# Performance work log

Hardware: AMD Instinct MI355X
Metric: run time of the kernel (lower is better)

The kernel has to match this reference:

```python
import jax, jax.numpy as jnp
import numpy as np

B, S, D = 2, 2048, 1024
H = 16
HD = D // H  # 64


def _xavier(key, shape):
    fan_out, fan_in = shape
    limit = np.sqrt(6.0 / (fan_in + fan_out)).astype(np.float32)
    return jax.random.uniform(key, shape, jnp.float32, -limit, limit)


def setup_inputs() -> dict:
    key = jax.random.key(0)
    ks = jax.random.split(key, 6)
    return {
        "x": jax.random.normal(ks[0], (B, S, D), jnp.float32),
        "pos_bias": jax.random.normal(ks[1], (1, H, S, S), jnp.float32) * 0.02,
        "sinusoidal_pos": jax.random.normal(ks[2], (1, 1, S, HD), jnp.float32),
        "mask": jax.random.randint(ks[3], (1, 1, S, S), 0, 2, jnp.int32),
        "W_qkv": _xavier(ks[4], (3 * D, D)),
        "b_qkv": jnp.zeros((3 * D,), jnp.float32),
        "W_o": _xavier(ks[5], (D, D)),
        "b_o": jnp.zeros((D,), jnp.float32),
    }


def _rotate_half(t):
    # t: [..., HD]; reshape to [..., 2, HD//2], swap halves with sign flip
    t2 = t.reshape(*t.shape[:-1], 2, HD // 2)
    a, b = t2[..., 0, :], t2[..., 1, :]
    return jnp.concatenate((-b, a), axis=-1)


def _apply_rope(t, sinusoidal_pos):
    sp = sinusoidal_pos[:, :, -t.shape[-2]:]
    return t * jnp.cos(sp) + _rotate_half(t) * jnp.sin(sp)


def reference(x, pos_bias, sinusoidal_pos, mask, W_qkv, b_qkv, W_o, b_o):
    b, s, _ = x.shape
    qkv = x @ W_qkv.T + b_qkv                     # [B,S,3D]
    qkv = qkv.reshape(b, s, H, 3 * HD).transpose(0, 2, 1, 3)  # [B,H,S,3hd]
    q, k, v = jnp.split(qkv, 3, axis=-1)
    q = _apply_rope(q, sinusoidal_pos)
    k = _apply_rope(k, sinusoidal_pos)
    logits = jnp.einsum("bhqd,bhkd->bhqk", q, k)  # [B,H,S,S]
    logits = (logits + pos_bias) / np.sqrt(HD).astype(np.float32)
    logits = jnp.where(mask == 0, jnp.float32(-9e15), logits)
    attn = jax.nn.softmax(logits, axis=-1)
    vals = jnp.einsum("bhqk,bhkd->bhqd", attn, v)
    vals = vals.transpose(0, 2, 1, 3).reshape(b, s, D)
    return vals @ W_o.T + b_o
```

## Files before the change

### kernel.cpp

```cpp
#include <hip/hip_runtime.h>
#include <cmath>

#define B_ 2
#define S_ 2048
#define D_ 1024
#define H_ 16
#define HD_ 64

typedef __attribute__((ext_vector_type(8))) short bf16x8;
typedef __attribute__((ext_vector_type(4))) short bf16x4;
typedef __attribute__((ext_vector_type(4))) float floatx4;
#define MFMA_BF16(a, b, c) __builtin_amdgcn_mfma_f32_16x16x32_bf16(a, b, c, 0, 0, 0)

#define QSCL 0.18033688011112042f

#if __has_builtin(__builtin_amdgcn_exp2f)
#define EXP2F(x) __builtin_amdgcn_exp2f(x)
#else
#define EXP2F(x) __expf((x) * 0.6931471805599453f)
#endif

__device__ __forceinline__ ushort f2bf(float x) {
    union { float f; unsigned u; } v; v.f = x;
    unsigned u = v.u;
    return (ushort)((u + 0x7FFFu + ((u >> 16) & 1u)) >> 16);
}
__device__ __forceinline__ float bf2f(ushort b) {
    union { unsigned u; float f; } v; v.u = ((unsigned)b) << 16;
    return v.f;
}
__device__ __forceinline__ unsigned cvt_pk_bf16(float a, float b) {
    unsigned r;
    asm("v_cvt_pk_bf16_f32 %0, %1, %2" : "=v"(r) : "v"(a), "v"(b));
    return r;
}

__global__ __launch_bounds__(256) void f32_split_bf16(
    const float* __restrict__ in, ushort* __restrict__ hi,
    ushort* __restrict__ lo, int n4)
{
    int i = blockIdx.x * 256 + threadIdx.x;
    if (i >= n4) return;
    float4 v = ((const float4*)in)[i];
    bf16x4 h, l;
    float vv[4] = {v.x, v.y, v.z, v.w};
#pragma unroll
    for (int j = 0; j < 4; ++j) {
        ushort hb = f2bf(vv[j]);
        h[j] = (short)hb;
        l[j] = (short)f2bf(vv[j] - bf2f(hb));
    }
    ((bf16x4*)hi)[i] = h;
    ((bf16x4*)lo)[i] = l;
}

__global__ __launch_bounds__(256, 2) void gemm_mfma_split(
    const ushort* __restrict__ Ah, const ushort* __restrict__ Al,
    const ushort* __restrict__ Wh, const ushort* __restrict__ Wl,
    const float* __restrict__ bias, float* __restrict__ C,
    int M, int N, int K)
{
    constexpr int LD = 40;
    __shared__ ushort Ash[128][LD], Asl[128][LD], Wsh[128][LD], Wsl[128][LD];

    const int tid = threadIdx.x;
    const int lane = tid & 63;
    const int wv = tid >> 6;
    const int l15 = lane & 15;
    const int quad = lane >> 4;
    const int bm = blockIdx.y * 128;
    const int bn = blockIdx.x * 128;
    const int mw = (wv & 1) * 64;
    const int nw = (wv >> 1) * 64;

    floatx4 acc[4][4];
#pragma unroll
    for (int i = 0; i < 4; ++i)
#pragma unroll
        for (int j = 0; j < 4; ++j) acc[i][j] = (floatx4){0.f, 0.f, 0.f, 0.f};

    const int srow = tid >> 2;
    const int sc8 = (tid & 3) * 8;

    bf16x8 pAh[2], pAl[2], pWh[2], pWl[2];
    auto fetch = [&](int k0) {
#pragma unroll
        for (int u = 0; u < 2; ++u) {
            int r = srow + u * 64;
            pAh[u] = *(const bf16x8*)(Ah + (size_t)(bm + r) * K + k0 + sc8);
            pAl[u] = *(const bf16x8*)(Al + (size_t)(bm + r) * K + k0 + sc8);
            pWh[u] = *(const bf16x8*)(Wh + (size_t)(bn + r) * K + k0 + sc8);
            pWl[u] = *(const bf16x8*)(Wl + (size_t)(bn + r) * K + k0 + sc8);
        }
    };

    fetch(0);
    for (int k0 = 0; k0 < K; k0 += 32) {
        __syncthreads();
#pragma unroll
        for (int u = 0; u < 2; ++u) {
            int r = srow + u * 64;
            *(bf16x8*)&Ash[r][sc8] = pAh[u];
            *(bf16x8*)&Asl[r][sc8] = pAl[u];
            *(bf16x8*)&Wsh[r][sc8] = pWh[u];
            *(bf16x8*)&Wsl[r][sc8] = pWl[u];
        }
        __syncthreads();
        if (k0 + 32 < K) fetch(k0 + 32);

        bf16x8 aH[4], aL[4], bH[4], bL[4];
#pragma unroll
        for (int f = 0; f < 4; ++f) {
            aH[f] = *(const bf16x8*)&Ash[mw + f * 16 + l15][quad * 8];
            aL[f] = *(const bf16x8*)&Asl[mw + f * 16 + l15][quad * 8];
            bH[f] = *(const bf16x8*)&Wsh[nw + f * 16 + l15][quad * 8];
            bL[f] = *(const bf16x8*)&Wsl[nw + f * 16 + l15][quad * 8];
        }
#pragma unroll
        for (int mf = 0; mf < 4; ++mf)
#pragma unroll
            for (int nf = 0; nf < 4; ++nf) {
                acc[mf][nf] = MFMA_BF16(aH[mf], bH[nf], acc[mf][nf]);
                acc[mf][nf] = MFMA_BF16(aH[mf], bL[nf], acc[mf][nf]);
                acc[mf][nf] = MFMA_BF16(aL[mf], bH[nf], acc[mf][nf]);
            }
    }

#pragma unroll
    for (int mf = 0; mf < 4; ++mf)
#pragma unroll
        for (int nf = 0; nf < 4; ++nf) {
            int col = bn + nw + nf * 16 + l15;
            float bv = bias[col];
#pragma unroll
            for (int reg = 0; reg < 4; ++reg) {
                int row = bm + mw + mf * 16 + quad * 4 + reg;
                C[(size_t)row * N + col] = acc[mf][nf][reg] + bv;
            }
        }
}

__global__ __launch_bounds__(256) void rope_split_bf16(
    const float* __restrict__ qkv, const float* __restrict__ sp,
    ushort* __restrict__ q_hi, ushort* __restrict__ q_lo,
    ushort* __restrict__ k_hi, ushort* __restrict__ k_lo,
    ushort* __restrict__ v_t)
{
    __shared__ ushort VT[64][72];
    const int s0 = blockIdx.x * 64;
    const int h = blockIdx.y;
    const int b = blockIdx.z;
    const int d = threadIdx.x & 63;
    const int sw = threadIdx.x >> 6;
    const float sgn = (d < 32) ? -1.f : 1.f;

#pragma unroll 4
    for (int i = 0; i < 16; ++i) {
        int sl = i * 4 + sw;
        int s = s0 + sl;
        size_t base = ((size_t)(b * S_ + s)) * (3 * D_) + h * (3 * HD_) + d;
        float tq = qkv[base];
        float tk = qkv[base + HD_];
        float tv = qkv[base + 2 * HD_];
        float spv = sp[s * HD_ + d];
        float c = cosf(spv), sn = sinf(spv);
        float pq = __shfl_xor(tq, 32);
        float pk = __shfl_xor(tk, 32);
        float qv = (tq * c + sgn * pq * sn) * QSCL;
        float kv = tk * c + sgn * pk * sn;

        size_t o = ((size_t)((b * H_ + h) * S_ + s)) * HD_ + d;
        ushort qh = f2bf(qv);
        q_hi[o] = qh; q_lo[o] = f2bf(qv - bf2f(qh));
        ushort kh = f2bf(kv);
        k_hi[o] = kh; k_lo[o] = f2bf(kv - bf2f(kh));
        VT[d][sl] = f2bf(tv);
    }
    __syncthreads();
    const int dd = threadIdx.x >> 2;
    const int c0 = (threadIdx.x & 3) * 16;
    size_t ob = ((size_t)((b * H_ + h) * HD_ + dd)) * S_ + s0 + c0;
    *(bf16x8*)(v_t + ob)     = *(const bf16x8*)&VT[dd][c0];
    *(bf16x8*)(v_t + ob + 8) = *(const bf16x8*)&VT[dd][c0 + 8];
}

__global__ __launch_bounds__(256, 2) void attn_flash_v4(
    const ushort* __restrict__ q_hi, const ushort* __restrict__ q_lo,
    const ushort* __restrict__ k_hi, const ushort* __restrict__ k_lo,
    const ushort* __restrict__ v_t, const float* __restrict__ pb,
    const int* __restrict__ mask,
    ushort* __restrict__ vals_hi, ushort* __restrict__ vals_lo)
{
    __shared__ ushort Kh[2][64][72];
    __shared__ ushort Kl[2][64][72];
    __shared__ ushort Vt[2][64][72];
    __shared__ ushort PBM[64][76];
    __shared__ ushort Ps[4][16][72];

    const int tid = threadIdx.x;
    const int lane = tid & 63;
    const int wv = tid >> 6;
    const int l15 = lane & 15;
    const int quad = lane >> 4;
    const int q0 = blockIdx.x * 64;
    const int h = blockIdx.y;
    const int qbase = q0 + wv * 16;

    bf16x8 qH0[2], qH1[2], qL0[2], qL1[2];
#pragma unroll
    for (int bb = 0; bb < 2; ++bb) {
        const size_t bh = ((size_t)(bb * H_ + h)) * (size_t)S_ * HD_;
        const ushort* qrh = q_hi + bh + (size_t)(qbase + l15) * HD_;
        const ushort* qrl = q_lo + bh + (size_t)(qbase + l15) * HD_;
        qH0[bb] = *(const bf16x8*)(qrh + quad * 8);
        qH1[bb] = *(const bf16x8*)(qrh + 32 + quad * 8);
        qL0[bb] = *(const bf16x8*)(qrl + quad * 8);
        qL1[bb] = *(const bf16x8*)(qrl + 32 + quad * 8);
    }

    floatx4 O4[2][4];
    float l_[2] = {0.f, 0.f};
#pragma unroll
    for (int bb = 0; bb < 2; ++bb)
#pragma unroll
        for (int f = 0; f < 4; ++f) O4[bb][f] = (floatx4){0.f, 0.f, 0.f, 0.f};

    const int kr = tid >> 3;
    const int kc8 = (tid & 7) * 8;
    const int pr = tid >> 4;
    const int pc4 = (tid & 15) * 4;

    bf16x8 pKh[2][2], pKl[2][2], pVt[2][2];
    float4 pPb[4];
    int4 pMk[4];
    auto fetch = [&](int kt) {
#pragma unroll
        for (int bb = 0; bb < 2; ++bb) {
            const size_t bh = ((size_t)(bb * H_ + h)) * (size_t)S_ * HD_;
#pragma unroll
            for (int u = 0; u < 2; ++u) {
                int r = kr + u * 32;
                pKh[bb][u] = *(const bf16x8*)(k_hi + bh + (size_t)(kt + r) * HD_ + kc8);
                pKl[bb][u] = *(const bf16x8*)(k_lo + bh + (size_t)(kt + r) * HD_ + kc8);
                pVt[bb][u] = *(const bf16x8*)(v_t + bh + (size_t)r * S_ + kt + kc8);
            }
        }
#pragma unroll
        for (int u = 0; u < 4; ++u) {
            int r = pr + u * 16;
            pPb[u] = *(const float4*)(pb + ((size_t)h * S_ + q0 + r) * S_ + kt + pc4);
            pMk[u] = *(const int4*)(mask + (size_t)(q0 + r) * S_ + kt + pc4);
        }
    };

    fetch(0);
    for (int kt = 0; kt < S_; kt += 64) {
        __syncthreads();
#pragma unroll
        for (int bb = 0; bb < 2; ++bb)
#pragma unroll
            for (int u = 0; u < 2; ++u) {
                int r = kr + u * 32;
                *(bf16x8*)&Kh[bb][r][kc8] = pKh[bb][u];
                *(bf16x8*)&Kl[bb][r][kc8] = pKl[bb][u];
                *(bf16x8*)&Vt[bb][r][kc8] = pVt[bb][u];
            }
#pragma unroll
        for (int u = 0; u < 4; ++u) {
            int r = pr + u * 16;
            float w0 = pMk[u].x == 0 ? -3e30f : pPb[u].x * QSCL;
            float w1 = pMk[u].y == 0 ? -3e30f : pPb[u].y * QSCL;
            float w2 = pMk[u].z == 0 ? -3e30f : pPb[u].z * QSCL;
            float w3 = pMk[u].w == 0 ? -3e30f : pPb[u].w * QSCL;
            uint2 rr;
            rr.x = cvt_pk_bf16(w0, w1);
            rr.y = cvt_pk_bf16(w2, w3);
            *(uint2*)&PBM[r][pc4] = rr;
        }
        __syncthreads();
        if (kt + 64 < S_) fetch(kt + 64);

        float pbv[4][4];
#pragma unroll
        for (int nf = 0; nf < 4; ++nf) {
            bf16x4 w = *(const bf16x4*)&PBM[wv * 16 + l15][nf * 16 + quad * 4];
#pragma unroll
            for (int reg = 0; reg < 4; ++reg) pbv[nf][reg] = bf2f((ushort)w[reg]);
        }

#pragma unroll
        for (int bb = 0; bb < 2; ++bb) {
            floatx4 S4[4];
            __builtin_amdgcn_s_setprio(1);
#pragma unroll
            for (int nf = 0; nf < 4; ++nf) {
                const int krow = nf * 16 + l15;
                bf16x8 bh0 = *(const bf16x8*)&Kh[bb][krow][quad * 8];
                bf16x8 bh1 = *(const bf16x8*)&Kh[bb][krow][32 + quad * 8];
                bf16x8 bl0 = *(const bf16x8*)&Kl[bb][krow][quad * 8];
                bf16x8 bl1 = *(const bf16x8*)&Kl[bb][krow][32 + quad * 8];
                floatx4 a = (floatx4){0.f, 0.f, 0.f, 0.f};
                a = MFMA_BF16(bh0, qH0[bb], a);
                a = MFMA_BF16(bh1, qH1[bb], a);
                a = MFMA_BF16(bl0, qH0[bb], a);
                a = MFMA_BF16(bl1, qH1[bb], a);
                a = MFMA_BF16(bh0, qL0[bb], a);
                a = MFMA_BF16(bh1, qL1[bb], a);
                S4[nf] = a;
            }
            __builtin_amdgcn_s_setprio(0);

#pragma unroll
            for (int nf = 0; nf < 4; ++nf) {
                float p[4];
#pragma unroll
                for (int reg = 0; reg < 4; ++reg) {
                    float x = S4[nf][reg] + pbv[nf][reg];
                    p[reg] = EXP2F(x);
                    l_[bb] += p[reg];
                }
                uint2 rr;
                rr.x = cvt_pk_bf16(p[0], p[1]);
                rr.y = cvt_pk_bf16(p[2], p[3]);
                *(uint2*)&Ps[wv][l15][nf * 16 + quad * 4] = rr;
            }

            bf16x8 pA0 = *(const bf16x8*)&Ps[wv][l15][quad * 8];
            bf16x8 pA1 = *(const bf16x8*)&Ps[wv][l15][32 + quad * 8];
            __builtin_amdgcn_s_setprio(1);
#pragma unroll
            for (int df = 0; df < 4; ++df) {
                const int vrow = df * 16 + l15;
                bf16x8 vB0 = *(const bf16x8*)&Vt[bb][vrow][quad * 8];
                bf16x8 vB1 = *(const bf16x8*)&Vt[bb][vrow][32 + quad * 8];
                O4[bb][df] = MFMA_BF16(pA0, vB0, O4[bb][df]);
                O4[bb][df] = MFMA_BF16(pA1, vB1, O4[bb][df]);
            }
            __builtin_amdgcn_s_setprio(0);
        }
    }

#pragma unroll
    for (int bb = 0; bb < 2; ++bb) {
        float lv = l_[bb];
        lv += __shfl_xor(lv, 16);
        lv += __shfl_xor(lv, 32);
        float linv = 1.f / lv;
#pragma unroll
        for (int reg = 0; reg < 4; ++reg) {
            float inv = __shfl(linv, quad * 4 + reg);
            const int row = qbase + quad * 4 + reg;
            size_t ob = ((size_t)(bb * S_ + row)) * D_ + h * HD_;
#pragma unroll
            for (int df = 0; df < 4; ++df) {
                float o = O4[bb][df][reg] * inv;
                ushort hb = f2bf(o);
                vals_hi[ob + df * 16 + l15] = hb;
                vals_lo[ob + df * 16 + l15] = f2bf(o - bf2f(hb));
            }
        }
    }
}

extern "C" void kernel_launch(void* const* d_in, const int* in_sizes, int n_in,
                              void* d_out, int out_size, void* d_ws, size_t ws_size,
                              hipStream_t stream) {
    const float* x      = (const float*)d_in[0];
    const float* pos_b  = (const float*)d_in[1];
    const float* sp     = (const float*)d_in[2];
    const int*   mask   = (const int*)d_in[3];
    const float* W_qkv  = (const float*)d_in[4];
    const float* b_qkv  = (const float*)d_in[5];
    const float* W_o    = (const float*)d_in[6];
    const float* b_o    = (const float*)d_in[7];
    float* out = (float*)d_out;

    char* w = (char*)d_ws;
    float*  qkv   = (float*)w;   w += (size_t)4096 * 3072 * 4;
    ushort* xv_hi = (ushort*)w;  w += (size_t)4096 * 1024 * 2;
    ushort* xv_lo = (ushort*)w;  w += (size_t)4096 * 1024 * 2;
    ushort* wq_hi = (ushort*)w;  w += (size_t)3072 * 1024 * 2;
    ushort* wq_lo = (ushort*)w;  w += (size_t)3072 * 1024 * 2;
    ushort* wo_hi = (ushort*)w;  w += (size_t)1024 * 1024 * 2;
    ushort* wo_lo = (ushort*)w;  w += (size_t)1024 * 1024 * 2;
    ushort* q_hi  = (ushort*)w;  w += (size_t)B_ * H_ * S_ * HD_ * 2;
    ushort* q_lo  = (ushort*)w;  w += (size_t)B_ * H_ * S_ * HD_ * 2;
    ushort* k_hi  = (ushort*)w;  w += (size_t)B_ * H_ * S_ * HD_ * 2;
    ushort* k_lo  = (ushort*)w;  w += (size_t)B_ * H_ * S_ * HD_ * 2;
    ushort* v_t   = (ushort*)w;  w += (size_t)B_ * H_ * S_ * HD_ * 2;

    f32_split_bf16<<<4096, 256, 0, stream>>>(x, xv_hi, xv_lo, 4096 * 1024 / 4);
    f32_split_bf16<<<3072, 256, 0, stream>>>(W_qkv, wq_hi, wq_lo, 3072 * 1024 / 4);
    f32_split_bf16<<<1024, 256, 0, stream>>>(W_o, wo_hi, wo_lo, 1024 * 1024 / 4);

    gemm_mfma_split<<<dim3(3072 / 128, 4096 / 128), 256, 0, stream>>>(
        xv_hi, xv_lo, wq_hi, wq_lo, b_qkv, qkv, 4096, 3072, 1024);

    rope_split_bf16<<<dim3(S_ / 64, H_, B_), 256, 0, stream>>>(
        qkv, sp, q_hi, q_lo, k_hi, k_lo, v_t);

    attn_flash_v4<<<dim3(S_ / 64, H_), 256, 0, stream>>>(
        q_hi, q_lo, k_hi, k_lo, v_t, pos_b, mask, xv_hi, xv_lo);

    gemm_mfma_split<<<dim3(1024 / 128, 4096 / 128), 256, 0, stream>>>(
        xv_hi, xv_lo, wo_hi, wo_lo, b_o, out, 4096, 1024, 1024);
}
```

Baseline: 629.8 us.

## Load K/V straight from global memory, drop LDS staging and barriers, swizzle blocks

The attention kernel no longer stages K, V and the bias/mask tile in shared memory. Each wave now loads K/V MFMA fragments directly from global memory and keeps only a per-thread register prefetch of its own bias/mask rows. This removes two __syncthreads per tile and most of the LDS footprint, which allows raising launch bounds to 3 blocks per SM. A block-index swizzle groups blocks of the same head onto nearby slots so K/V are reused in cache. The trade-off is redundant global/L2 traffic, since all 4 waves and neighbouring blocks re-read the same K/V tiles with less coalesced access.

```diff
diff --git a/kernel.cpp b/kernel.cpp
--- a/kernel.cpp
+++ b/kernel.cpp
@@ -184,17 +184,13 @@
     *(bf16x8*)(v_t + ob + 8) = *(const bf16x8*)&VT[dd][c0 + 8];
 }
 
-__global__ __launch_bounds__(256, 2) void attn_flash_v4(
+__global__ __launch_bounds__(256, 3) void attn_flash_v5(
     const ushort* __restrict__ q_hi, const ushort* __restrict__ q_lo,
     const ushort* __restrict__ k_hi, const ushort* __restrict__ k_lo,
     const ushort* __restrict__ v_t, const float* __restrict__ pb,
     const int* __restrict__ mask,
     ushort* __restrict__ vals_hi, ushort* __restrict__ vals_lo)
 {
-    __shared__ ushort Kh[2][64][72];
-    __shared__ ushort Kl[2][64][72];
-    __shared__ ushort Vt[2][64][72];
-    __shared__ ushort PBM[64][76];
     __shared__ ushort Ps[4][16][72];
 
     const int tid = threadIdx.x;
@@ -202,16 +198,21 @@
     const int wv = tid >> 6;
     const int l15 = lane & 15;
     const int quad = lane >> 4;
-    const int q0 = blockIdx.x * 64;
-    const int h = blockIdx.y;
+
+    const int flat = (int)blockIdx.x + (int)blockIdx.y * (S_ / 64);
+    const int swz = (flat & 7) * 64 + (flat >> 3);
+    const int q0 = (swz & 31) * 64;
+    const int h = swz >> 5;
     const int qbase = q0 + wv * 16;
 
+    const size_t bstride = (size_t)H_ * S_ * HD_;
+    const size_t bh = (size_t)h * S_ * HD_;
+
     bf16x8 qH0[2], qH1[2], qL0[2], qL1[2];
 #pragma unroll
     for (int bb = 0; bb < 2; ++bb) {
-        const size_t bh = ((size_t)(bb * H_ + h)) * (size_t)S_ * HD_;
-        const ushort* qrh = q_hi + bh + (size_t)(qbase + l15) * HD_;
-        const ushort* qrl = q_lo + bh + (size_t)(qbase + l15) * HD_;
+        const ushort* qrh = q_hi + bh + bb * bstride + (size_t)(qbase + l15) * HD_;
+        const ushort* qrl = q_lo + bh + bb * bstride + (size_t)(qbase + l15) * HD_;
         qH0[bb] = *(const bf16x8*)(qrh + quad * 8);
         qH1[bb] = *(const bf16x8*)(qrh + 32 + quad * 8);
         qL0[bb] = *(const bf16x8*)(qrl + quad * 8);
@@ -225,87 +226,55 @@
 #pragma unroll
         for (int f = 0; f < 4; ++f) O4[bb][f] = (floatx4){0.f, 0.f, 0.f, 0.f};
 
-    const int kr = tid >> 3;
-    const int kc8 = (tid & 7) * 8;
-    const int pr = tid >> 4;
-    const int pc4 = (tid & 15) * 4;
-
-    bf16x8 pKh[2][2], pKl[2][2], pVt[2][2];
+    const float* pbrow = pb + ((size_t)h * S_ + (size_t)(qbase + l15)) * S_ + quad * 4;
+    const int* mkrow = mask + (size_t)(qbase + l15) * S_ + quad * 4;
+
     float4 pPb[4];
     int4 pMk[4];
-    auto fetch = [&](int kt) {
+    auto fetchPB = [&](int kt) {
+#pragma unroll
+        for (int nf = 0; nf < 4; ++nf) {
+            pPb[nf] = *(const float4*)(pbrow + kt + nf * 16);
+            pMk[nf] = *(const int4*)(mkrow + kt + nf * 16);
+        }
+    };
+
+    fetchPB(0);
+    for (int kt = 0; kt < S_; kt += 64) {
+        float pbv[4][4];
+#pragma unroll
+        for (int nf = 0; nf < 4; ++nf) {
+            const float* pf = (const float*)&pPb[nf];
+            const int* mf = (const int*)&pMk[nf];
+#pragma unroll
+            for (int reg = 0; reg < 4; ++reg)
+                pbv[nf][reg] = (mf[reg] == 0) ? -3e30f : pf[reg] * QSCL;
+        }
+        if (kt + 64 < S_) fetchPB(kt + 64);
+
 #pragma unroll
         for (int bb = 0; bb < 2; ++bb) {
-            const size_t bh = ((size_t)(bb * H_ + h)) * (size_t)S_ * HD_;
-#pragma unroll
-            for (int u = 0; u < 2; ++u) {
-                int r = kr + u * 32;
-                pKh[bb][u] = *(const bf16x8*)(k_hi + bh + (size_t)(kt + r) * HD_ + kc8);
-                pKl[bb][u] = *(const bf16x8*)(k_lo + bh + (size_t)(kt + r) * HD_ + kc8);
-                pVt[bb][u] = *(const bf16x8*)(v_t + bh + (size_t)r * S_ + kt + kc8);
-            }
-        }
-#pragma unroll
-        for (int u = 0; u < 4; ++u) {
-            int r = pr + u * 16;
-            pPb[u] = *(const float4*)(pb + ((size_t)h * S_ + q0 + r) * S_ + kt + pc4);
-            pMk[u] = *(const int4*)(mask + (size_t)(q0 + r) * S_ + kt + pc4);
-        }
-    };
-
-    fetch(0);
-    for (int kt = 0; kt < S_; kt += 64) {
-        __syncthreads();
-#pragma unroll
-        for (int bb = 0; bb < 2; ++bb)
-#pragma unroll
-            for (int u = 0; u < 2; ++u) {
-                int r = kr + u * 32;
-                *(bf16x8*)&Kh[bb][r][kc8] = pKh[bb][u];
-                *(bf16x8*)&Kl[bb][r][kc8] = pKl[bb][u];
-                *(bf16x8*)&Vt[bb][r][kc8] = pVt[bb][u];
-            }
-#pragma unroll
-        for (int u = 0; u < 4; ++u) {
-            int r = pr + u * 16;
-            float w0 = pMk[u].x == 0 ? -3e30f : pPb[u].x * QSCL;
-            float w1 = pMk[u].y == 0 ? -3e30f : pPb[u].y * QSCL;
-            float w2 = pMk[u].z == 0 ? -3e30f : pPb[u].z * QSCL;
-            float w3 = pMk[u].w == 0 ? -3e30f : pPb[u].w * QSCL;
-            uint2 rr;
-            rr.x = cvt_pk_bf16(w0, w1);
-            rr.y = cvt_pk_bf16(w2, w3);
-            *(uint2*)&PBM[r][pc4] = rr;
-        }
-        __syncthreads();
-        if (kt + 64 < S_) fetch(kt + 64);
-
-        float pbv[4][4];
-#pragma unroll
-        for (int nf = 0; nf < 4; ++nf) {
-            bf16x4 w = *(const bf16x4*)&PBM[wv * 16 + l15][nf * 16 + quad * 4];
-#pragma unroll
-            for (int reg = 0; reg < 4; ++reg) pbv[nf][reg] = bf2f((ushort)w[reg]);
-        }
-
-#pragma unroll
-        for (int bb = 0; bb < 2; ++bb) {
+            const ushort* kh = k_hi + bh + bb * bstride + (size_t)kt * HD_;
+            const ushort* kl = k_lo + bh + bb * bstride + (size_t)kt * HD_;
+            const ushort* vt = v_t + bh + bb * bstride + kt;
+
             floatx4 S4[4];
             __builtin_amdgcn_s_setprio(1);
 #pragma unroll
             for (int nf = 0; nf < 4; ++nf) {
-                const int krow = nf * 16 + l15;
-                bf16x8 bh0 = *(const bf16x8*)&Kh[bb][krow][quad * 8];
-                bf16x8 bh1 = *(const bf16x8*)&Kh[bb][krow][32 + quad * 8];
-                bf16x8 bl0 = *(const bf16x8*)&Kl[bb][krow][quad * 8];
-                bf16x8 bl1 = *(const bf16x8*)&Kl[bb][krow][32 + quad * 8];
+                const ushort* krh = kh + (size_t)(nf * 16 + l15) * HD_;
+                const ushort* krl = kl + (size_t)(nf * 16 + l15) * HD_;
+                bf16x8 kh0 = *(const bf16x8*)(krh + quad * 8);
+                bf16x8 kh1 = *(const bf16x8*)(krh + 32 + quad * 8);
+                bf16x8 kl0 = *(const bf16x8*)(krl + quad * 8);
+                bf16x8 kl1 = *(const bf16x8*)(krl + 32 + quad * 8);
                 floatx4 a = (floatx4){0.f, 0.f, 0.f, 0.f};
-                a = MFMA_BF16(bh0, qH0[bb], a);
-                a = MFMA_BF16(bh1, qH1[bb], a);
-                a = MFMA_BF16(bl0, qH0[bb], a);
-                a = MFMA_BF16(bl1, qH1[bb], a);
-                a = MFMA_BF16(bh0, qL0[bb], a);
-                a = MFMA_BF16(bh1, qL1[bb], a);
+                a = MFMA_BF16(kh0, qH0[bb], a);
+                a = MFMA_BF16(kh1, qH1[bb], a);
+                a = MFMA_BF16(kl0, qH0[bb], a);
+                a = MFMA_BF16(kl1, qH1[bb], a);
+                a = MFMA_BF16(kh0, qL0[bb], a);
+                a = MFMA_BF16(kh1, qL1[bb], a);
                 S4[nf] = a;
             }
             __builtin_amdgcn_s_setprio(0);
@@ -330,9 +299,9 @@
             __builtin_amdgcn_s_setprio(1);
 #pragma unroll
             for (int df = 0; df < 4; ++df) {
-                const int vrow = df * 16 + l15;
-                bf16x8 vB0 = *(const bf16x8*)&Vt[bb][vrow][quad * 8];
-                bf16x8 vB1 = *(const bf16x8*)&Vt[bb][vrow][32 + quad * 8];
+                const ushort* vrow = vt + (size_t)(df * 16 + l15) * S_;
+                bf16x8 vB0 = *(const bf16x8*)(vrow + quad * 8);
+                bf16x8 vB1 = *(const bf16x8*)(vrow + 32 + quad * 8);
                 O4[bb][df] = MFMA_BF16(pA0, vB0, O4[bb][df]);
                 O4[bb][df] = MFMA_BF16(pA1, vB1, O4[bb][df]);
             }
@@ -399,7 +368,7 @@
     rope_split_bf16<<<dim3(S_ / 64, H_, B_), 256, 0, stream>>>(
         qkv, sp, q_hi, q_lo, k_hi, k_lo, v_t);
 
-    attn_flash_v4<<<dim3(S_ / 64, H_), 256, 0, stream>>>(
+    attn_flash_v5<<<dim3(S_ / 64, H_), 256, 0, stream>>>(
         q_hi, q_lo, k_hi, k_lo, v_t, pos_b, mask, xv_hi, xv_lo);
 
     gemm_mfma_split<<<dim3(1024 / 128, 4096 / 128), 256, 0, stream>>>(
```

After: 999.4 us. 1.59x slower.
